# Kernel tuning notes

Hardware: AMD Instinct MI355X
Metric: run time of the kernel (lower is better)

The kernel has to match this reference:

```python
import jax, jax.numpy as jnp
import numpy as np

V, E, U, B, T = 32000, 256, 512, 64, 256  # vocab, embed_dim, enc_units, batch, seq_len


def setup_inputs() -> dict:
    key = jax.random.key(0)
    ks = jax.random.split(key, 8)
    x = jax.random.randint(ks[0], (B, T), 0, V)  # int ids; 0 = mask token
    emb = jax.random.normal(ks[1], (V, E), dtype=jnp.float32) * 0.02
    W_f = jax.random.normal(ks[2], (E, 4 * U), dtype=jnp.float32) * 0.05
    R_f = jax.random.normal(ks[3], (U, 4 * U), dtype=jnp.float32) * 0.05
    b_f = jnp.zeros((4 * U,), dtype=jnp.float32)
    W_b = jax.random.normal(ks[4], (E, 4 * U), dtype=jnp.float32) * 0.05
    R_b = jax.random.normal(ks[5], (U, 4 * U), dtype=jnp.float32) * 0.05
    b_b = jnp.zeros((4 * U,), dtype=jnp.float32)
    return {"x": x, "emb": emb, "W_f": W_f, "R_f": R_f, "b_f": b_f,
            "W_b": W_b, "R_b": R_b, "b_b": b_b}


def _lstm_scan(e_seq, m_seq, W, R, b):
    # e_seq: [T,B,E], m_seq: [T,B,1] bool. Keras LSTM with recurrent_activation='tanh':
    # i,f,o gates use tanh (non-default!), candidate and cell-output use tanh.
    x_proj = jnp.einsum('tbe,eg->tbg', e_seq, W) + b  # precompute input projection [T,B,4U]
    h0 = jnp.zeros((e_seq.shape[1], U), dtype=e_seq.dtype)
    c0 = jnp.zeros_like(h0)

    def step(carry, inp):
        h, c = carry
        xz, m = inp
        z = xz + h @ R  # [B,4U]
        zi, zf, zg, zo = jnp.split(z, 4, axis=-1)
        i = jnp.tanh(zi)
        f = jnp.tanh(zf)
        g = jnp.tanh(zg)
        o = jnp.tanh(zo)
        c_new = f * c + i * g
        h_new = o * jnp.tanh(c_new)
        # Keras masking: masked steps carry previous state/output through
        h = jnp.where(m, h_new, h)
        c = jnp.where(m, c_new, c)
        return (h, c), h

    (hT, cT), hs = jax.lax.scan(step, (h0, c0), (x_proj, m_seq))
    return hs, hT  # [T,B,U], [B,U]


def reference(x, emb, W_f, R_f, b_f, W_b, R_b, b_b):
    mask = (x != 0)  # mask_zero=True
    e = emb[x]                      # [B,T,E] embedding lookup
    e_t = jnp.swapaxes(e, 0, 1)     # [T,B,E]
    m_t = jnp.swapaxes(mask, 0, 1)[:, :, None]  # [T,B,1]
    # forward direction
    h_fwd, _ = _lstm_scan(e_t, m_t, W_f, R_f, b_f)
    # backward direction: reverse time, scan, reverse outputs back (Keras Bidirectional)
    h_bwd_rev, backward_h = _lstm_scan(e_t[::-1], m_t[::-1], W_b, R_b, b_b)
    h_bwd = h_bwd_rev[::-1]
    final_output = jnp.swapaxes(jnp.concatenate([h_fwd, h_bwd], axis=-1), 0, 1)  # [B,T,2U]
    return final_output, backward_h
```

## Files before the change

kernel.cpp:

```cpp
#include <hip/hip_runtime.h>

#define V_ 32000
#define E_ 256
#define U_ 512
#define B_ 64
#define T_ 256
#define G_ 2048

#define RSTR 516
#define ASTR 260
#define WESTR 132


#define GLDS16(gsrc, ldst) __builtin_amdgcn_global_load_lds( \
    (const __attribute__((address_space(1))) void*)(gsrc),    \
    (__attribute__((address_space(3))) void*)(ldst), 16, 0, 0)

__global__ __launch_bounds__(512, 1)
void bilstm_kernel(const int* __restrict__ x,
                   const float* __restrict__ emb,
                   const float* __restrict__ Wf, const float* __restrict__ Rf,
                   const float* __restrict__ bf,
                   const float* __restrict__ Wb, const float* __restrict__ Rb,
                   const float* __restrict__ bb,
                   float* __restrict__ out, float* __restrict__ hbuf,
                   unsigned* __restrict__ bar, float* __restrict__ xz,
                   int CH)
{
    __shared__ __align__(16) float Rl[32 * RSTR];
    __shared__ __align__(16) float HA[64 * ASTR];
    __shared__ __align__(16) float Wel[32 * WESTR];

    const int blk = blockIdx.x;
    const int dir = blk >> 7;
    const int rem = blk & 127;
    const int u0 = (rem >> 1) * 8;
    const int b0base = (rem & 1) * 32;
    const int grp = dir * 2 + (rem & 1);
    const int mem = rem >> 1;
    unsigned* myslot = bar + (grp * 64 + mem) * 16;

    const int tid   = threadIdx.x;
    const int wv    = tid >> 6;
    const int lane  = tid & 63;
    const int uu    = lane & 7;
    const int blgrp = lane >> 3;
    const int blf   = tid >> 3;
    const int fuu   = tid & 7;

    const float* Wd = dir ? Wb : Wf;
    const float* Rd = dir ? Rb : Rf;
    const float* bd = dir ? bb : bf;

    {
        const int sgc  = tid & 31;
        const int gcol = ((sgc >> 3) * 512) + u0 + (sgc & 7);
        for (int k = tid >> 5; k < 512; k += 16)
            Rl[sgc * RSTR + k] = Rd[(size_t)k * G_ + gcol];
    }
    float bias4[4];
    #pragma unroll
    for (int g = 0; g < 4; ++g) bias4[g] = bd[g * 512 + u0 + fuu];

    float c_reg = 0.0f;
    const float4* Rl4  = reinterpret_cast<const float4*>(Rl);
    const float4* HA4  = reinterpret_cast<const float4*>(HA);
    const float4* Wel4 = reinterpret_cast<const float4*>(Wel);
    float4* HAw4 = reinterpret_cast<float4*>(HA);
    float4* P4s = reinterpret_cast<float4*>(Wel);
    float4* P4p = reinterpret_cast<float4*>(HA);

    __syncthreads();

    const int nch = T_ / CH;
    for (int ch = 0; ch < nch; ++ch) {
        const int nat = CH >> 1;
        for (int at = 0; at < nat; ++at) {
            __syncthreads();
            for (int i = 0; i < 8; ++i) {
                int rr   = wv * 8 + i;
                int tloc = at * 2 + (rr >> 5);
                int bla  = rr & 31;
                int sg   = ch * CH + tloc;
                int tea  = dir ? (T_ - 1 - sg) : sg;
                int tok  = x[(b0base + bla) * T_ + tea];
                GLDS16(emb + (size_t)tok * E_ + lane * 4, HA + rr * ASTR);
            }
            float pacc[8][4];
            #pragma unroll
            for (int j = 0; j < 8; ++j)
                #pragma unroll
                for (int g = 0; g < 4; ++g) pacc[j][g] = 0.0f;

            for (int kh = 0; kh < 2; ++kh) {
                if (kh) __syncthreads();
                {
                    const int sgc  = tid & 31;
                    const int gcol = ((sgc >> 3) * 512) + u0 + (sgc & 7);
                    for (int kk = tid >> 5; kk < 128; kk += 16)
                        Wel[sgc * WESTR + kk] = Wd[(size_t)(kh * 128 + kk) * G_ + gcol];
                }
                __syncthreads();
                #pragma unroll
                for (int k4 = 0; k4 < 4; ++k4) {
                    const int kw = wv * 4 + k4;
                    float4 w0 = Wel4[(0 * 8 + uu) * 33 + kw];
                    float4 w1 = Wel4[(1 * 8 + uu) * 33 + kw];
                    float4 w2 = Wel4[(2 * 8 + uu) * 33 + kw];
                    float4 w3 = Wel4[(3 * 8 + uu) * 33 + kw];
                    #pragma unroll
                    for (int j = 0; j < 8; ++j) {
                        float4 a = HA4[(blgrp + 8 * j) * 65 + kh * 32 + kw];
                        pacc[j][0] = fmaf(w0.x,a.x,pacc[j][0]); pacc[j][0] = fmaf(w0.y,a.y,pacc[j][0]);
                        pacc[j][0] = fmaf(w0.z,a.z,pacc[j][0]); pacc[j][0] = fmaf(w0.w,a.w,pacc[j][0]);
                        pacc[j][1] = fmaf(w1.x,a.x,pacc[j][1]); pacc[j][1] = fmaf(w1.y,a.y,pacc[j][1]);
                        pacc[j][1] = fmaf(w1.z,a.z,pacc[j][1]); pacc[j][1] = fmaf(w1.w,a.w,pacc[j][1]);
                        pacc[j][2] = fmaf(w2.x,a.x,pacc[j][2]); pacc[j][2] = fmaf(w2.y,a.y,pacc[j][2]);
                        pacc[j][2] = fmaf(w2.z,a.z,pacc[j][2]); pacc[j][2] = fmaf(w2.w,a.w,pacc[j][2]);
                        pacc[j][3] = fmaf(w3.x,a.x,pacc[j][3]); pacc[j][3] = fmaf(w3.y,a.y,pacc[j][3]);
                        pacc[j][3] = fmaf(w3.z,a.z,pacc[j][3]); pacc[j][3] = fmaf(w3.w,a.w,pacc[j][3]);
                    }
                }
            }
            __syncthreads();
            #pragma unroll
            for (int j = 0; j < 8; ++j)
                P4p[(wv * 64 + blgrp + 8 * j) * 8 + uu] =
                    float4{pacc[j][0], pacc[j][1], pacc[j][2], pacc[j][3]};
            __syncthreads();
            {
                const int r   = tid >> 3;
                const int uq  = tid & 7;
                const int tl  = at * 2 + (r >> 5);
                const int bla = r & 31;
                float* dst = xz + ((size_t)blk * CH + tl) * 1024;
                float4 s = P4p[(0 * 64 + r) * 8 + uq];
                #pragma unroll
                for (int q = 1; q < 8; ++q) {
                    float4 p = P4p[(q * 64 + r) * 8 + uq];
                    s.x += p.x; s.y += p.y; s.z += p.z; s.w += p.w;
                }
                dst[(0 * 8 + uq) * 32 + bla] = s.x;
                dst[(1 * 8 + uq) * 32 + bla] = s.y;
                dst[(2 * 8 + uq) * 32 + bla] = s.z;
                dst[(3 * 8 + uq) * 32 + bla] = s.w;
            }
        }
        __syncthreads();

        for (int sc = 0; sc < CH; ++sc) {
            const int s   = ch * CH + sc;
            const int te  = dir ? (T_ - 1 - s) : s;
            const int cur = s & 1, nxt = cur ^ 1;

            int mtok = 0;
            float xzv[4] = {0.f, 0.f, 0.f, 0.f};
            if (tid < 256) {
                mtok = x[(b0base + blf) * T_ + te];
                const float* xzp = xz + ((size_t)blk * CH + sc) * 1024;
                #pragma unroll
                for (int g = 0; g < 4; ++g)
                    xzv[g] = xzp[(g * 8 + fuu) * 32 + blf] + bias4[g];
            }

            if (s > 0) {
                if (tid < 64) {
                    unsigned* slot = bar + (grp * 64 + tid) * 16;
                    while (__hip_atomic_load(slot, __ATOMIC_RELAXED,
                                             __HIP_MEMORY_SCOPE_AGENT) < (unsigned)s)
                        __builtin_amdgcn_s_sleep(1);
                }
                __syncthreads();
            }

            {
                const char* hsrc = (const char*)(hbuf +
                    ((size_t)(cur * 2 + dir) * B_ + b0base) * U_);
                #pragma unroll
                for (int i = 0; i < 8; ++i) {
                    int off16 = (wv * 8 + i) * 64 + lane;
                    int row   = off16 >> 7;
                    int col4  = off16 & 127;
                    const unsigned long long* p =
                        (const unsigned long long*)(hsrc + (size_t)off16 * 16);
                    unsigned long long a = __hip_atomic_load(p,     __ATOMIC_RELAXED,
                                                             __HIP_MEMORY_SCOPE_AGENT);
                    unsigned long long b = __hip_atomic_load(p + 1, __ATOMIC_RELAXED,
                                                             __HIP_MEMORY_SCOPE_AGENT);
                    float2 fa = __builtin_bit_cast(float2, a);
                    float2 fb = __builtin_bit_cast(float2, b);
                    HAw4[row * 129 + col4] = float4{fa.x, fa.y, fb.x, fb.y};
                }
            }
            __syncthreads();

            float pz[4][4];
            #pragma unroll
            for (int j = 0; j < 4; ++j)
                #pragma unroll
                for (int g = 0; g < 4; ++g) pz[j][g] = 0.0f;
            const int kbase = wv * 16;
            #pragma unroll 4
            for (int k4 = 0; k4 < 16; ++k4) {
                const int kk = kbase + k4;
                float4 h0 = HA4[(blgrp + 8 * 0) * 129 + kk];
                float4 h1 = HA4[(blgrp + 8 * 1) * 129 + kk];
                float4 h2 = HA4[(blgrp + 8 * 2) * 129 + kk];
                float4 h3 = HA4[(blgrp + 8 * 3) * 129 + kk];
                #pragma unroll
                for (int g = 0; g < 4; ++g) {
                    float4 w = Rl4[(g * 8 + uu) * 129 + kk];
                    pz[0][g] = fmaf(w.x,h0.x,pz[0][g]); pz[0][g] = fmaf(w.y,h0.y,pz[0][g]);
                    pz[0][g] = fmaf(w.z,h0.z,pz[0][g]); pz[0][g] = fmaf(w.w,h0.w,pz[0][g]);
                    pz[1][g] = fmaf(w.x,h1.x,pz[1][g]); pz[1][g] = fmaf(w.y,h1.y,pz[1][g]);
                    pz[1][g] = fmaf(w.z,h1.z,pz[1][g]); pz[1][g] = fmaf(w.w,h1.w,pz[1][g]);
                    pz[2][g] = fmaf(w.x,h2.x,pz[2][g]); pz[2][g] = fmaf(w.y,h2.y,pz[2][g]);
                    pz[2][g] = fmaf(w.z,h2.z,pz[2][g]); pz[2][g] = fmaf(w.w,h2.w,pz[2][g]);
                    pz[3][g] = fmaf(w.x,h3.x,pz[3][g]); pz[3][g] = fmaf(w.y,h3.y,pz[3][g]);
                    pz[3][g] = fmaf(w.z,h3.z,pz[3][g]); pz[3][g] = fmaf(w.w,h3.w,pz[3][g]);
                }
            }
            float h_old = (tid < 256) ? HA[blf * RSTR + u0 + fuu] : 0.0f;

            if (wv >= 4) {
                #pragma unroll
                for (int j = 0; j < 4; ++j)
                    P4s[((wv - 4) * 32 + blgrp + 8 * j) * 8 + uu] =
                        float4{pz[j][0], pz[j][1], pz[j][2], pz[j][3]};
            }
            __syncthreads();
            if (wv < 4) {
                #pragma unroll
                for (int j = 0; j < 4; ++j) {
                    const int idx = (wv * 32 + blgrp + 8 * j) * 8 + uu;
                    float4 t = P4s[idx];
                    t.x += pz[j][0]; t.y += pz[j][1];
                    t.z += pz[j][2]; t.w += pz[j][3];
                    P4s[idx] = t;
                }
            }
            __syncthreads();

            if (tid < 256) {
                float4 z0 = P4s[(0 * 32 + blf) * 8 + fuu];
                float4 z1 = P4s[(1 * 32 + blf) * 8 + fuu];
                float4 z2 = P4s[(2 * 32 + blf) * 8 + fuu];
                float4 z3 = P4s[(3 * 32 + blf) * 8 + fuu];
                float fi = tanhf(z0.x + z1.x + z2.x + z3.x + xzv[0]);
                float ff = tanhf(z0.y + z1.y + z2.y + z3.y + xzv[1]);
                float fg = tanhf(z0.z + z1.z + z2.z + z3.z + xzv[2]);
                float fo = tanhf(z0.w + z1.w + z2.w + z3.w + xzv[3]);
                float cn = fmaf(ff, c_reg, fi * fg);
                float hn = fo * tanhf(cn);
                bool  m  = (mtok != 0);
                float hsel = m ? hn : h_old;
                c_reg = m ? cn : c_reg;

                const int b = b0base + blf;
                __hip_atomic_store(&hbuf[((size_t)(nxt * 2 + dir) * B_ + b) * U_ + u0 + fuu],
                                   hsel, __ATOMIC_RELAXED, __HIP_MEMORY_SCOPE_AGENT);
                out[((size_t)b * T_ + te) * 1024 + dir * 512 + u0 + fuu] = hsel;
                if (dir == 1 && s == T_ - 1)
                    out[(size_t)B_ * T_ * 1024 + (size_t)b * U_ + u0 + fuu] = hsel;
            }

            __syncthreads();
            if (tid == 0)
                __hip_atomic_store(myslot, (unsigned)(s + 1), __ATOMIC_RELAXED,
                                   __HIP_MEMORY_SCOPE_AGENT);
        }
    }
}

extern "C" void kernel_launch(void* const* d_in, const int* in_sizes, int n_in,
                              void* d_out, int out_size, void* d_ws, size_t ws_size,
                              hipStream_t stream) {
    const int*   x   = (const int*)d_in[0];
    const float* emb = (const float*)d_in[1];
    const float* Wf  = (const float*)d_in[2];
    const float* Rf  = (const float*)d_in[3];
    const float* bfp = (const float*)d_in[4];
    const float* Wb  = (const float*)d_in[5];
    const float* Rb  = (const float*)d_in[6];
    const float* bbp = (const float*)d_in[7];
    float* out  = (float*)d_out;
    float* hbuf = (float*)d_ws;
    unsigned* bar = (unsigned*)((char*)d_ws + 512 * 1024);
    float* xzbuf  = (float*)((char*)d_ws + (1 << 20));

    int CH = 32;
    while (CH > 2 && (size_t)(CH + 1) * (1 << 20) > ws_size) CH >>= 1;

    hipMemsetAsync(hbuf, 0, (size_t)2 * B_ * U_ * sizeof(float), stream);
    hipMemsetAsync(bar, 0, 4 * 64 * 16 * sizeof(unsigned), stream);

    void* args[] = {
        (void*)&x, (void*)&emb,
        (void*)&Wf, (void*)&Rf, (void*)&bfp,
        (void*)&Wb, (void*)&Rb, (void*)&bbp,
        (void*)&out, (void*)&hbuf, (void*)&bar, (void*)&xzbuf, (void*)&CH
    };
    hipLaunchCooperativeKernel((const void*)bilstm_kernel,
                               dim3(256), dim3(512), args, 0, stream);
}
```

Baseline: 3.384 ms.

## Restructure recurrent matvec with per-lane k-split, DPP reductions and per-wave barrier polling

Remaps threads so each wave handles 8 batch rows with lanes splitting the reduction dimension. Each lane loads four weight float4s and reuses them across eight hidden rows, using XOR-swizzled column indices to avoid LDS bank conflicts. Partial sums are combined with DPP lane shuffles instead of an LDS partial-sum pass, which removes one __syncthreads and the cross-wave accumulation step. Every wave now polls the inter-block barrier itself rather than one wave polling followed by a block barrier. The cost is higher register pressure from 32 accumulators and redundant polling traffic from all waves.

```diff
diff --git a/kernel.cpp b/kernel.cpp
--- a/kernel.cpp
+++ b/kernel.cpp
@@ -15,6 +15,17 @@
 #define GLDS16(gsrc, ldst) __builtin_amdgcn_global_load_lds( \
     (const __attribute__((address_space(1))) void*)(gsrc),    \
     (__attribute__((address_space(3))) void*)(ldst), 16, 0, 0)
+
+__device__ __forceinline__ float dpp_sum8(float v) {
+    int t;
+    t = __builtin_amdgcn_update_dpp(0, __float_as_int(v), 0xB1, 0xF, 0xF, true);
+    v += __int_as_float(t);
+    t = __builtin_amdgcn_update_dpp(0, __float_as_int(v), 0x4E, 0xF, 0xF, true);
+    v += __int_as_float(t);
+    t = __builtin_amdgcn_update_dpp(0, __float_as_int(v), 0x104, 0xF, 0xF, true);
+    v += __int_as_float(t);
+    return v;
+}
 
 __global__ __launch_bounds__(512, 1)
 void bilstm_kernel(const int* __restrict__ x,
@@ -45,8 +56,14 @@
     const int lane  = tid & 63;
     const int uu    = lane & 7;
     const int blgrp = lane >> 3;
-    const int blf   = tid >> 3;
-    const int fuu   = tid & 7;
+    const int ksl    = lane & 7;
+    const int ct     = lane >> 3;
+    const int rt     = wv >> 1;
+    const int kshalf = wv & 1;
+    const int ks     = kshalf * 8 + ksl;
+    const int jf     = kshalf * 4 + ksl;
+    const int row_f  = rt * 8 + jf;
+    const bool fin   = (ksl < 4);
 
     const float* Wd = dir ? Wb : Wf;
     const float* Rd = dir ? Rb : Rf;
@@ -60,7 +77,7 @@
     }
     float bias4[4];
     #pragma unroll
-    for (int g = 0; g < 4; ++g) bias4[g] = bd[g * 512 + u0 + fuu];
+    for (int g = 0; g < 4; ++g) bias4[g] = bd[g * 512 + u0 + ct];
 
     float c_reg = 0.0f;
     const float4* Rl4  = reinterpret_cast<const float4*>(Rl);
@@ -154,23 +171,20 @@
             const int cur = s & 1, nxt = cur ^ 1;
 
             int mtok = 0;
-            float xzv[4] = {0.f, 0.f, 0.f, 0.f};
-            if (tid < 256) {
-                mtok = x[(b0base + blf) * T_ + te];
+            float xzv4[4] = {0.f, 0.f, 0.f, 0.f};
+            if (fin) {
+                mtok = x[(b0base + row_f) * T_ + te];
                 const float* xzp = xz + ((size_t)blk * CH + sc) * 1024;
                 #pragma unroll
                 for (int g = 0; g < 4; ++g)
-                    xzv[g] = xzp[(g * 8 + fuu) * 32 + blf] + bias4[g];
+                    xzv4[g] = xzp[(g * 8 + ct) * 32 + row_f] + bias4[g];
             }
 
             if (s > 0) {
-                if (tid < 64) {
-                    unsigned* slot = bar + (grp * 64 + tid) * 16;
-                    while (__hip_atomic_load(slot, __ATOMIC_RELAXED,
-                                             __HIP_MEMORY_SCOPE_AGENT) < (unsigned)s)
-                        __builtin_amdgcn_s_sleep(1);
-                }
-                __syncthreads();
+                unsigned* slot = bar + (grp * 64 + lane) * 16;
+                while (__hip_atomic_load(slot, __ATOMIC_RELAXED,
+                                         __HIP_MEMORY_SCOPE_AGENT) < (unsigned)s)
+                    __builtin_amdgcn_s_sleep(1);
             }
 
             {
@@ -194,74 +208,67 @@
             }
             __syncthreads();
 
-            float pz[4][4];
-            #pragma unroll
-            for (int j = 0; j < 4; ++j)
+            float pz[8][4];
+            #pragma unroll
+            for (int j = 0; j < 8; ++j)
                 #pragma unroll
                 for (int g = 0; g < 4; ++g) pz[j][g] = 0.0f;
-            const int kbase = wv * 16;
-            #pragma unroll 4
-            for (int k4 = 0; k4 < 16; ++k4) {
-                const int kk = kbase + k4;
-                float4 h0 = HA4[(blgrp + 8 * 0) * 129 + kk];
-                float4 h1 = HA4[(blgrp + 8 * 1) * 129 + kk];
-                float4 h2 = HA4[(blgrp + 8 * 2) * 129 + kk];
-                float4 h3 = HA4[(blgrp + 8 * 3) * 129 + kk];
-                #pragma unroll
-                for (int g = 0; g < 4; ++g) {
-                    float4 w = Rl4[(g * 8 + uu) * 129 + kk];
-                    pz[0][g] = fmaf(w.x,h0.x,pz[0][g]); pz[0][g] = fmaf(w.y,h0.y,pz[0][g]);
-                    pz[0][g] = fmaf(w.z,h0.z,pz[0][g]); pz[0][g] = fmaf(w.w,h0.w,pz[0][g]);
-                    pz[1][g] = fmaf(w.x,h1.x,pz[1][g]); pz[1][g] = fmaf(w.y,h1.y,pz[1][g]);
-                    pz[1][g] = fmaf(w.z,h1.z,pz[1][g]); pz[1][g] = fmaf(w.w,h1.w,pz[1][g]);
-                    pz[2][g] = fmaf(w.x,h2.x,pz[2][g]); pz[2][g] = fmaf(w.y,h2.y,pz[2][g]);
-                    pz[2][g] = fmaf(w.z,h2.z,pz[2][g]); pz[2][g] = fmaf(w.w,h2.w,pz[2][g]);
-                    pz[3][g] = fmaf(w.x,h3.x,pz[3][g]); pz[3][g] = fmaf(w.y,h3.y,pz[3][g]);
-                    pz[3][g] = fmaf(w.z,h3.z,pz[3][g]); pz[3][g] = fmaf(w.w,h3.w,pz[3][g]);
-                }
-            }
-            float h_old = (tid < 256) ? HA[blf * RSTR + u0 + fuu] : 0.0f;
-
-            if (wv >= 4) {
-                #pragma unroll
-                for (int j = 0; j < 4; ++j)
-                    P4s[((wv - 4) * 32 + blgrp + 8 * j) * 8 + uu] =
+            const int hbase = (rt * 8) * 129 + ks * 8;
+            const int rbase = ct * 129 + ks * 8;
+            #pragma unroll
+            for (int i = 0; i < 8; ++i) {
+                const int c = i ^ ksl;
+                float4 w0 = Rl4[rbase + 0 * 1032 + c];
+                float4 w1 = Rl4[rbase + 1 * 1032 + c];
+                float4 w2 = Rl4[rbase + 2 * 1032 + c];
+                float4 w3 = Rl4[rbase + 3 * 1032 + c];
+                #pragma unroll
+                for (int j = 0; j < 8; ++j) {
+                    float4 h = HA4[hbase + j * 129 + c];
+                    pz[j][0] = fmaf(w0.x,h.x,pz[j][0]); pz[j][0] = fmaf(w0.y,h.y,pz[j][0]);
+                    pz[j][0] = fmaf(w0.z,h.z,pz[j][0]); pz[j][0] = fmaf(w0.w,h.w,pz[j][0]);
+                    pz[j][1] = fmaf(w1.x,h.x,pz[j][1]); pz[j][1] = fmaf(w1.y,h.y,pz[j][1]);
+                    pz[j][1] = fmaf(w1.z,h.z,pz[j][1]); pz[j][1] = fmaf(w1.w,h.w,pz[j][1]);
+                    pz[j][2] = fmaf(w2.x,h.x,pz[j][2]); pz[j][2] = fmaf(w2.y,h.y,pz[j][2]);
+                    pz[j][2] = fmaf(w2.z,h.z,pz[j][2]); pz[j][2] = fmaf(w2.w,h.w,pz[j][2]);
+                    pz[j][3] = fmaf(w3.x,h.x,pz[j][3]); pz[j][3] = fmaf(w3.y,h.y,pz[j][3]);
+                    pz[j][3] = fmaf(w3.z,h.z,pz[j][3]); pz[j][3] = fmaf(w3.w,h.w,pz[j][3]);
+                }
+            }
+            float h_old = fin ? HA[row_f * RSTR + u0 + ct] : 0.0f;
+
+            #pragma unroll
+            for (int j = 0; j < 8; ++j)
+                #pragma unroll
+                for (int g = 0; g < 4; ++g) pz[j][g] = dpp_sum8(pz[j][g]);
+
+            #pragma unroll
+            for (int j = 0; j < 8; ++j) {
+                if (ksl == (j & 3))
+                    P4s[(((rt * 2 + kshalf) * 8) + j) * 8 + ct] =
                         float4{pz[j][0], pz[j][1], pz[j][2], pz[j][3]};
             }
             __syncthreads();
-            if (wv < 4) {
-                #pragma unroll
-                for (int j = 0; j < 4; ++j) {
-                    const int idx = (wv * 32 + blgrp + 8 * j) * 8 + uu;
-                    float4 t = P4s[idx];
-                    t.x += pz[j][0]; t.y += pz[j][1];
-                    t.z += pz[j][2]; t.w += pz[j][3];
-                    P4s[idx] = t;
-                }
-            }
-            __syncthreads();
-
-            if (tid < 256) {
-                float4 z0 = P4s[(0 * 32 + blf) * 8 + fuu];
-                float4 z1 = P4s[(1 * 32 + blf) * 8 + fuu];
-                float4 z2 = P4s[(2 * 32 + blf) * 8 + fuu];
-                float4 z3 = P4s[(3 * 32 + blf) * 8 + fuu];
-                float fi = tanhf(z0.x + z1.x + z2.x + z3.x + xzv[0]);
-                float ff = tanhf(z0.y + z1.y + z2.y + z3.y + xzv[1]);
-                float fg = tanhf(z0.z + z1.z + z2.z + z3.z + xzv[2]);
-                float fo = tanhf(z0.w + z1.w + z2.w + z3.w + xzv[3]);
+
+            if (fin) {
+                float4 z0 = P4s[(((rt * 2 + 0) * 8) + jf) * 8 + ct];
+                float4 z1 = P4s[(((rt * 2 + 1) * 8) + jf) * 8 + ct];
+                float fi = tanhf(z0.x + z1.x + xzv4[0]);
+                float ff = tanhf(z0.y + z1.y + xzv4[1]);
+                float fg = tanhf(z0.z + z1.z + xzv4[2]);
+                float fo = tanhf(z0.w + z1.w + xzv4[3]);
                 float cn = fmaf(ff, c_reg, fi * fg);
                 float hn = fo * tanhf(cn);
                 bool  m  = (mtok != 0);
                 float hsel = m ? hn : h_old;
                 c_reg = m ? cn : c_reg;
 
-                const int b = b0base + blf;
-                __hip_atomic_store(&hbuf[((size_t)(nxt * 2 + dir) * B_ + b) * U_ + u0 + fuu],
+                const int b = b0base + row_f;
+                __hip_atomic_store(&hbuf[((size_t)(nxt * 2 + dir) * B_ + b) * U_ + u0 + ct],
                                    hsel, __ATOMIC_RELAXED, __HIP_MEMORY_SCOPE_AGENT);
-                out[((size_t)b * T_ + te) * 1024 + dir * 512 + u0 + fuu] = hsel;
+                out[((size_t)b * T_ + te) * 1024 + dir * 512 + u0 + ct] = hsel;
                 if (dir == 1 && s == T_ - 1)
-                    out[(size_t)B_ * T_ * 1024 + (size_t)b * U_ + u0 + fuu] = hsel;
+                    out[(size_t)B_ * T_ * 1024 + (size_t)b * U_ + u0 + ct] = hsel;
             }
 
             __syncthreads();
```

Result: slower. 9.726 ms (+187.4%).
